# Kernel optimization log

Measured on AMD Instinct MI355X. Metric: run time of the kernel, lower is better.

The kernel has to match this reference:

```python
import jax, jax.numpy as jnp
import numpy as np
import math

# ---- HashGridEncoder constants (from init_kwargs) ----
L = 16            # levels
LOG2T = 19
T = 1 << LOG2T    # hash table size per level
F = 2             # features per entry
N_MIN = 16
N_MAX = 2048
N_PTS = 524288    # number of query points
BB_MIN = np.zeros(3, np.float32)
BB_MAX = np.ones(3, np.float32)
B = math.exp((math.log(N_MAX) - math.log(N_MIN)) / (L - 1))
RES = np.array([math.floor(N_MIN * B ** i) for i in range(L)], dtype=np.float32)  # per-level grid resolution
VERTS = np.array([[0,0,0],[0,0,1],[0,1,0],[0,1,1],[1,0,0],[1,0,1],[1,1,0],[1,1,1]], dtype=np.int32)  # 8 cube corners
PI = np.array([1, 2654435761, 805459861], dtype=np.uint32)  # spatial hash primes
MASK = np.uint32((1 << 19) - 1)  # hard-coded mask from source


def setup_inputs() -> dict:
    key = jax.random.key(0)
    k1, k2 = jax.random.split(key)
    xyz = jax.random.uniform(k1, (N_PTS, 3), dtype=jnp.float32)  # points inside bbox [0,1]^3
    # nn.init.uniform_(weight, -1e-4, 1e-4)
    tables = jax.random.uniform(k2, (L, T, F), minval=-1e-4, maxval=1e-4, dtype=jnp.float32)
    return {"xyz": xyz, "tables": tables}


def reference(xyz, tables):
    # cell size per level: (bb_max - bb_min) / resolution  -> [L,3]
    cell = (BB_MAX - BB_MIN)[None, :] / RES[:, None]
    # normalized grid coords for all levels at once: [L,N,3]
    u = (xyz[None, :, :] - BB_MIN) / cell[:, None, :]
    mi = jnp.floor(u).astype(jnp.int32)            # min corner index [L,N,3]
    d = u - mi.astype(jnp.float32)                 # trilinear fracs == (xyz - min_vertex)/cell, [L,N,3]
    # 8 corner integer coords: [L,N,8,3]; uint32 wrapping matches int64-mul + low-19-bit mask
    corners = (mi[:, :, None, :] + VERTS[None, None]).astype(jnp.uint32)
    h = (corners[..., 0] * PI[0]) ^ (corners[..., 1] * PI[1]) ^ (corners[..., 2] * PI[2])
    h = (h & MASK).astype(jnp.int32)               # hash indices [L,N,8], all < T
    # gather all levels in one flat lookup
    flat = tables.reshape(L * T, F)
    idx = h + (jnp.arange(L, dtype=jnp.int32) * T)[:, None, None]
    emb = flat[idx]                                # [L,N,8,F]
    # trilinear weights: prod over axes of d (corner bit 1) or 1-d (corner bit 0) -> [L,N,8]
    w = jnp.prod(jnp.where(VERTS[None, None].astype(bool), d[:, :, None, :], 1.0 - d[:, :, None, :]), axis=-1)
    c = jnp.einsum('lnv,lnvf->lnf', w, emb)        # interpolated features [L,N,F]
    # torch.cat(embedded, dim=-1): level-major concat -> [N, L*F]
    return jnp.moveaxis(c, 0, 1).reshape(xyz.shape[0], L * F)
```

## Files before the change

### kernel.cpp

```cpp
#include <hip/hip_runtime.h>
#include <cmath>

#define NLEVELS 16
#define TBL     (1u << 19)
#define HMASK   0x7FFFFu
#define NPTS    524288

typedef float v4f __attribute__((ext_vector_type(4)));

struct LevelParams {
    float cell[NLEVELS];
};

__device__ __forceinline__ void ngp_hash(
    float x, float y, float z, float cell, unsigned* __restrict__ h,
    float& dx, float& dy, float& dz)
{
    const float ux = x / cell;
    const float uy = y / cell;
    const float uz = z / cell;
    const float fx = floorf(ux);
    const float fy = floorf(uy);
    const float fz = floorf(uz);
    dx = ux - fx;
    dy = uy - fy;
    dz = uz - fz;

    const unsigned ix = (unsigned)(int)fx;
    const unsigned iy = (unsigned)(int)fy;
    const unsigned iz = (unsigned)(int)fz;

    const unsigned hx0 = ix;
    const unsigned hx1 = ix + 1u;
    const unsigned hy0 = iy * 2654435761u;
    const unsigned hy1 = (iy + 1u) * 2654435761u;
    const unsigned hz0 = iz * 805459861u;
    const unsigned hz1 = (iz + 1u) * 805459861u;

    h[0] = (hx0 ^ hy0 ^ hz0) & HMASK;
    h[1] = (hx0 ^ hy0 ^ hz1) & HMASK;
    h[2] = (hx0 ^ hy1 ^ hz0) & HMASK;
    h[3] = (hx0 ^ hy1 ^ hz1) & HMASK;
    h[4] = (hx1 ^ hy0 ^ hz0) & HMASK;
    h[5] = (hx1 ^ hy0 ^ hz1) & HMASK;
    h[6] = (hx1 ^ hy1 ^ hz0) & HMASK;
    h[7] = (hx1 ^ hy1 ^ hz1) & HMASK;
}

__device__ __forceinline__ void ngp_weights(
    float dx, float dy, float dz, float* __restrict__ w)
{
    const float wx0 = 1.0f - dx;
    const float wy0 = 1.0f - dy;
    const float wz0 = 1.0f - dz;
    const float p00 = wx0 * wy0;
    const float p01 = wx0 * dy;
    const float p10 = dx * wy0;
    const float p11 = dx * dy;
    w[0] = p00 * wz0;
    w[1] = p00 * dz;
    w[2] = p01 * wz0;
    w[3] = p01 * dz;
    w[4] = p10 * wz0;
    w[5] = p10 * dz;
    w[6] = p11 * wz0;
    w[7] = p11 * dz;
}

__device__ __forceinline__ float2 ngp_combine(
    const float* __restrict__ w, const float2* __restrict__ e)
{
    float c0 = w[0] * e[0].x;
    float c1 = w[0] * e[0].y;
    #pragma unroll
    for (int c = 1; c < 8; ++c) {
        c0 += w[c] * e[c].x;
        c1 += w[c] * e[c].y;
    }
    return make_float2(c0, c1);
}

__global__ __launch_bounds__(256) void ngp_phase1(
    const float* __restrict__ xyz,
    const float* __restrict__ tables,
    float2* __restrict__ ws,
    LevelParams lp)
{
    const unsigned b = blockIdx.x;
    const int level = (int)(((b >> 13) << 3) | (b & 7u));
    const int chunk = (int)((b >> 3) & 1023u);
    const int n0 = chunk * 512 + threadIdx.x;
    const int n1 = n0 + 256;

    const float x0 = xyz[3 * n0 + 0];
    const float y0 = xyz[3 * n0 + 1];
    const float z0 = xyz[3 * n0 + 2];
    const float x1 = xyz[3 * n1 + 0];
    const float y1 = xyz[3 * n1 + 1];
    const float z1 = xyz[3 * n1 + 2];

    const float cell = lp.cell[level];
    const float2* __restrict__ tab = (const float2*)tables + ((size_t)level << 19);

    unsigned h0[8], h1[8];
    float dx0, dy0, dz0, dx1, dy1, dz1;
    ngp_hash(x0, y0, z0, cell, h0, dx0, dy0, dz0);
    ngp_hash(x1, y1, z1, cell, h1, dx1, dy1, dz1);

    float2 e0[8], e1[8];
    #pragma unroll
    for (int c = 0; c < 8; ++c) e0[c] = tab[h0[c]];
    #pragma unroll
    for (int c = 0; c < 8; ++c) e1[c] = tab[h1[c]];

    float w0[8], w1[8];
    ngp_weights(dx0, dy0, dz0, w0);
    ngp_weights(dx1, dy1, dz1, w1);

    const float2 r0 = ngp_combine(w0, e0);
    const float2 r1 = ngp_combine(w1, e1);

    ws[(size_t)level * NPTS + n0] = r0;
    ws[(size_t)level * NPTS + n1] = r1;
}

#define P2STRIDE 258

__global__ __launch_bounds__(256) void ngp_phase2(
    const float2* __restrict__ ws,
    float* __restrict__ out)
{
    __shared__ float2 lds[NLEVELS * P2STRIDE];
    const unsigned base = blockIdx.x * 256;
    const unsigned tid = threadIdx.x;

    #pragma unroll
    for (int l = 0; l < NLEVELS; ++l)
        lds[l * P2STRIDE + tid] = ws[(size_t)l * NPTS + base + tid];

    __syncthreads();

    #pragma unroll
    for (int it = 0; it < 8; ++it) {
        const unsigned j = it * 256 + tid;
        const unsigned nl = j >> 3;
        const unsigned k = j & 7u;
        const float2 a = lds[(2u * k)      * P2STRIDE + nl];
        const float2 b = lds[(2u * k + 1u) * P2STRIDE + nl];
        v4f v = { a.x, a.y, b.x, b.y };
        *(v4f*)(out + (size_t)base * 32 + (size_t)j * 4) = v;
    }
}

__global__ __launch_bounds__(256) void ngp_encode(
    const float* __restrict__ xyz,
    const float* __restrict__ tables,
    float* __restrict__ out,
    LevelParams lp)
{
    const int n = blockIdx.x * 256 + threadIdx.x;
    const float x = xyz[3 * n + 0];
    const float y = xyz[3 * n + 1];
    const float z = xyz[3 * n + 2];

    float acc[2 * NLEVELS];
    const float2* __restrict__ tab_base = (const float2*)tables;

    #pragma unroll
    for (int l = 0; l < NLEVELS; ++l) {
        unsigned h[8];
        float dx, dy, dz;
        ngp_hash(x, y, z, lp.cell[l], h, dx, dy, dz);
        const float2* __restrict__ tab = tab_base + ((size_t)l << 19);
        float2 e[8];
        #pragma unroll
        for (int c = 0; c < 8; ++c) e[c] = tab[h[c]];
        float w[8];
        ngp_weights(dx, dy, dz, w);
        const float2 r = ngp_combine(w, e);
        acc[2 * l + 0] = r.x;
        acc[2 * l + 1] = r.y;
    }

    v4f* o4 = (v4f*)(out + (size_t)n * 32);
    #pragma unroll
    for (int j = 0; j < 8; ++j) {
        v4f v = { acc[4 * j + 0], acc[4 * j + 1],
                  acc[4 * j + 2], acc[4 * j + 3] };
        o4[j] = v;
    }
}

extern "C" void kernel_launch(void* const* d_in, const int* in_sizes, int n_in,
                              void* d_out, int out_size, void* d_ws, size_t ws_size,
                              hipStream_t stream) {
    const float* xyz    = (const float*)d_in[0];
    const float* tables = (const float*)d_in[1];
    float* out          = (float*)d_out;

    LevelParams lp;
    const double B = std::exp((std::log(2048.0) - std::log(16.0)) / 15.0);
    for (int i = 0; i < NLEVELS; ++i) {
        const double r = std::floor(16.0 * std::pow(B, (double)i));
        lp.cell[i] = 1.0f / (float)r;
    }

    const size_t ws_needed = (size_t)NLEVELS * NPTS * sizeof(float2);

    if (ws_size >= ws_needed) {
        float2* ws = (float2*)d_ws;
        hipLaunchKernelGGL(ngp_phase1, dim3(NLEVELS * (NPTS / 512)), dim3(256), 0, stream,
                           xyz, tables, ws, lp);
        hipLaunchKernelGGL(ngp_phase2, dim3(NPTS / 256), dim3(256), 0, stream,
                           ws, out);
    } else {
        hipLaunchKernelGGL(ngp_encode, dim3(NPTS / 256), dim3(256), 0, stream,
                           xyz, tables, out, lp);
    }
}
```

Measured before the change: 405.0 us.

## Morton-bucket sort points before hash-grid gather to improve table locality

Adds a counting sort of query points into 32^3 Morton buckets (count, scan, scatter kernels) and runs the per-level gather on the spatially sorted points. Phase 2 then scatters the results back to original order through a permutation, and phase 1 drops to one point per thread. The goal is that neighbouring threads hit nearby hash entries on the coarse levels, which raises cache reuse of the gathers. In exchange it adds three kernels, a memset, atomics, a serial single-block scan, and non-contiguous output writes. Fine levels hash randomly anyway, so the locality gain is limited to the coarse levels.

Result: faster. 377.9 us (-6.7%).

```diff
diff --git a/kernel.cpp b/kernel.cpp
--- a/kernel.cpp
+++ b/kernel.cpp
@@ -2,15 +2,27 @@
 #include <cmath>
 
 #define NLEVELS 16
-#define TBL     (1u << 19)
 #define HMASK   0x7FFFFu
 #define NPTS    524288
+#define NBUCKET 32768
 
 typedef float v4f __attribute__((ext_vector_type(4)));
 
 struct LevelParams {
     float cell[NLEVELS];
 };
+
+__device__ __forceinline__ unsigned spread5(unsigned v) {
+    return (v & 1u) | ((v & 2u) << 2) | ((v & 4u) << 4) |
+           ((v & 8u) << 6) | ((v & 16u) << 8);
+}
+
+__device__ __forceinline__ unsigned morton_key(float x, float y, float z) {
+    unsigned bx = min(31u, (unsigned)(x * 32.0f));
+    unsigned by = min(31u, (unsigned)(y * 32.0f));
+    unsigned bz = min(31u, (unsigned)(z * 32.0f));
+    return spread5(bx) | (spread5(by) << 1) | (spread5(bz) << 2);
+}
 
 __device__ __forceinline__ void ngp_hash(
     float x, float y, float z, float cell, unsigned* __restrict__ h,
@@ -80,75 +92,120 @@
     return make_float2(c0, c1);
 }
 
+__global__ __launch_bounds__(256) void bucket_count(
+    const float* __restrict__ xyz, unsigned* __restrict__ counts)
+{
+    const int n = blockIdx.x * 256 + threadIdx.x;
+    const float x = xyz[3 * n + 0];
+    const float y = xyz[3 * n + 1];
+    const float z = xyz[3 * n + 2];
+    atomicAdd(&counts[morton_key(x, y, z)], 1u);
+}
+
+__global__ __launch_bounds__(1024) void bucket_scan(
+    const unsigned* __restrict__ counts, unsigned* __restrict__ cursor)
+{
+    __shared__ unsigned psum[1024];
+    const unsigned t = threadIdx.x;
+
+    unsigned s = 0;
+    for (int i = 0; i < 32; ++i) s += counts[t * 32 + i];
+    psum[t] = s;
+    __syncthreads();
+
+    for (unsigned off = 1; off < 1024; off <<= 1) {
+        unsigned v = 0;
+        if (t >= off) v = psum[t - off];
+        __syncthreads();
+        if (t >= off) psum[t] += v;
+        __syncthreads();
+    }
+
+    unsigned excl = psum[t] - s;
+    for (int i = 0; i < 32; ++i) {
+        cursor[t * 32 + i] = excl;
+        excl += counts[t * 32 + i];
+    }
+}
+
+__global__ __launch_bounds__(256) void bucket_scatter(
+    const float* __restrict__ xyz, unsigned* __restrict__ cursor,
+    unsigned* __restrict__ perm, float* __restrict__ xyz_sorted)
+{
+    const int n = blockIdx.x * 256 + threadIdx.x;
+    const float x = xyz[3 * n + 0];
+    const float y = xyz[3 * n + 1];
+    const float z = xyz[3 * n + 2];
+    const unsigned key = morton_key(x, y, z);
+    const unsigned p = atomicAdd(&cursor[key], 1u);
+    perm[p] = (unsigned)n;
+    xyz_sorted[3 * p + 0] = x;
+    xyz_sorted[3 * p + 1] = y;
+    xyz_sorted[3 * p + 2] = z;
+}
+
 __global__ __launch_bounds__(256) void ngp_phase1(
-    const float* __restrict__ xyz,
+    const float* __restrict__ xyz_sorted,
     const float* __restrict__ tables,
     float2* __restrict__ ws,
     LevelParams lp)
 {
     const unsigned b = blockIdx.x;
-    const int level = (int)(((b >> 13) << 3) | (b & 7u));
-    const int chunk = (int)((b >> 3) & 1023u);
-    const int n0 = chunk * 512 + threadIdx.x;
-    const int n1 = n0 + 256;
-
-    const float x0 = xyz[3 * n0 + 0];
-    const float y0 = xyz[3 * n0 + 1];
-    const float z0 = xyz[3 * n0 + 2];
-    const float x1 = xyz[3 * n1 + 0];
-    const float y1 = xyz[3 * n1 + 1];
-    const float z1 = xyz[3 * n1 + 2];
+    const int level = (int)(((b >> 14) << 3) | (b & 7u));
+    const int chunk = (int)((b >> 3) & 2047u);
+    const int p = chunk * 256 + threadIdx.x;
+
+    const float x = xyz_sorted[3 * p + 0];
+    const float y = xyz_sorted[3 * p + 1];
+    const float z = xyz_sorted[3 * p + 2];
 
     const float cell = lp.cell[level];
     const float2* __restrict__ tab = (const float2*)tables + ((size_t)level << 19);
 
-    unsigned h0[8], h1[8];
-    float dx0, dy0, dz0, dx1, dy1, dz1;
-    ngp_hash(x0, y0, z0, cell, h0, dx0, dy0, dz0);
-    ngp_hash(x1, y1, z1, cell, h1, dx1, dy1, dz1);
-
-    float2 e0[8], e1[8];
-    #pragma unroll
-    for (int c = 0; c < 8; ++c) e0[c] = tab[h0[c]];
-    #pragma unroll
-    for (int c = 0; c < 8; ++c) e1[c] = tab[h1[c]];
-
-    float w0[8], w1[8];
-    ngp_weights(dx0, dy0, dz0, w0);
-    ngp_weights(dx1, dy1, dz1, w1);
-
-    const float2 r0 = ngp_combine(w0, e0);
-    const float2 r1 = ngp_combine(w1, e1);
-
-    ws[(size_t)level * NPTS + n0] = r0;
-    ws[(size_t)level * NPTS + n1] = r1;
-}
-
-#define P2STRIDE 258
+    unsigned h[8];
+    float dx, dy, dz;
+    ngp_hash(x, y, z, cell, h, dx, dy, dz);
+
+    float2 e[8];
+    #pragma unroll
+    for (int c = 0; c < 8; ++c) e[c] = tab[h[c]];
+
+    float w[8];
+    ngp_weights(dx, dy, dz, w);
+
+    const float2 r = ngp_combine(w, e);
+
+    ws[(size_t)level * NPTS + p] = r;
+}
+
+#define P2S 257
 
 __global__ __launch_bounds__(256) void ngp_phase2(
     const float2* __restrict__ ws,
+    const unsigned* __restrict__ perm,
     float* __restrict__ out)
 {
-    __shared__ float2 lds[NLEVELS * P2STRIDE];
+    __shared__ float2 lds[NLEVELS * P2S];
+    __shared__ unsigned nperm[256];
     const unsigned base = blockIdx.x * 256;
-    const unsigned tid = threadIdx.x;
-
+    const unsigned t = threadIdx.x;
+
+    nperm[t] = perm[base + t];
     #pragma unroll
     for (int l = 0; l < NLEVELS; ++l)
-        lds[l * P2STRIDE + tid] = ws[(size_t)l * NPTS + base + tid];
+        lds[l * P2S + t] = ws[(size_t)l * NPTS + base + t];
 
     __syncthreads();
 
     #pragma unroll
     for (int it = 0; it < 8; ++it) {
-        const unsigned j = it * 256 + tid;
-        const unsigned nl = j >> 3;
+        const unsigned j = it * 256 + t;
+        const unsigned pl = j >> 3;
         const unsigned k = j & 7u;
-        const float2 a = lds[(2u * k)      * P2STRIDE + nl];
-        const float2 b = lds[(2u * k + 1u) * P2STRIDE + nl];
+        const float2 a = lds[(2u * k)      * P2S + pl];
+        const float2 b = lds[(2u * k + 1u) * P2S + pl];
         v4f v = { a.x, a.y, b.x, b.y };
-        *(v4f*)(out + (size_t)base * 32 + (size_t)j * 4) = v;
+        *(v4f*)(out + (size_t)nperm[pl] * 32 + k * 4) = v;
     }
 }
 
@@ -205,14 +262,32 @@
         lp.cell[i] = 1.0f / (float)r;
     }
 
-    const size_t ws_needed = (size_t)NLEVELS * NPTS * sizeof(float2);
+    const size_t off_feat   = 0;
+    const size_t off_xyzs   = off_feat + (size_t)NLEVELS * NPTS * sizeof(float2);
+    const size_t off_perm   = off_xyzs + (size_t)NPTS * 3 * sizeof(float);
+    const size_t off_counts = off_perm + (size_t)NPTS * sizeof(unsigned);
+    const size_t off_cursor = off_counts + (size_t)NBUCKET * sizeof(unsigned);
+    const size_t ws_needed  = off_cursor + (size_t)NBUCKET * sizeof(unsigned);
 
     if (ws_size >= ws_needed) {
-        float2* ws = (float2*)d_ws;
-        hipLaunchKernelGGL(ngp_phase1, dim3(NLEVELS * (NPTS / 512)), dim3(256), 0, stream,
-                           xyz, tables, ws, lp);
+        char* wsb = (char*)d_ws;
+        float2*   ws_feat    = (float2*)(wsb + off_feat);
+        float*    xyz_sorted = (float*)(wsb + off_xyzs);
+        unsigned* perm       = (unsigned*)(wsb + off_perm);
+        unsigned* counts     = (unsigned*)(wsb + off_counts);
+        unsigned* cursor     = (unsigned*)(wsb + off_cursor);
+
+        hipMemsetAsync(counts, 0, NBUCKET * sizeof(unsigned), stream);
+        hipLaunchKernelGGL(bucket_count, dim3(NPTS / 256), dim3(256), 0, stream,
+                           xyz, counts);
+        hipLaunchKernelGGL(bucket_scan, dim3(1), dim3(1024), 0, stream,
+                           counts, cursor);
+        hipLaunchKernelGGL(bucket_scatter, dim3(NPTS / 256), dim3(256), 0, stream,
+                           xyz, cursor, perm, xyz_sorted);
+        hipLaunchKernelGGL(ngp_phase1, dim3(NLEVELS * (NPTS / 256)), dim3(256), 0, stream,
+                           xyz_sorted, tables, ws_feat, lp);
         hipLaunchKernelGGL(ngp_phase2, dim3(NPTS / 256), dim3(256), 0, stream,
-                           ws, out);
+                           ws_feat, perm, out);
     } else {
         hipLaunchKernelGGL(ngp_encode, dim3(NPTS / 256), dim3(256), 0, stream,
                            xyz, tables, out, lp);
```
